# Performance work log

Measured on AMD Instinct MI355X. Metric: run time of the kernel, lower is better.

The kernel has to match this reference:

```python
import math
import jax, jax.numpy as jnp
import numpy as np

B, H, W = 32, 32, 32
SQRT2 = 1.4142  # literal from the torch module


def setup_inputs() -> dict:
    key = jax.random.key(0)
    k1, k2, k3 = jax.random.split(key, 3)
    cost_maps = jax.random.uniform(k1, (B, 1, H, W), jnp.float32, 0.5, 1.5)
    si = jax.random.randint(k2, (B,), 0, H * W)
    gi = jax.random.randint(k3, (B,), 0, H * W)
    gi = jnp.where(gi == si, (gi + 1) % (H * W), gi)
    start_maps = jax.nn.one_hot(si, H * W, dtype=jnp.float32).reshape(B, 1, H, W)
    goal_maps = jax.nn.one_hot(gi, H * W, dtype=jnp.float32).reshape(B, 1, H, W)
    return {"cost_maps": cost_maps, "start_maps": start_maps, "goal_maps": goal_maps}


def _st_softmax_noexp(val):
    # straight-through softmax-without-exp: soft normalize, hard argmax one-hot
    b = val.shape[0]
    v = val.reshape(b, -1)
    y = v / v.sum(-1, keepdims=True)
    ind = jnp.argmax(y, -1)
    y_hard = jax.nn.one_hot(ind, v.shape[-1], dtype=y.dtype)
    y = jax.lax.stop_gradient(y_hard - y) + y
    return y.reshape(val.shape)


def _conv3x3(x, k):
    # x: [B,H,W], k: [3,3]; torch F.conv2d is cross-correlation, as is lax conv
    return jax.lax.conv_general_dilated(x[:, None], k[None, None], (1, 1), ((1, 1), (1, 1)))[:, 0]


def _forward(cost_maps, start_maps, goal_maps, w=1.0):
    cm = cost_maps[:, 0]
    sm = start_maps[:, 0]
    gm = goal_maps[:, 0]
    obs = cm  # obstacles_maps defaults to cost_maps
    b, hgt, wid = cm.shape
    hw = hgt * wid

    # Euclidean heuristic (dis_type='Euc'), scaled by cost map and weight w
    loc = jnp.stack(jnp.meshgrid(jnp.arange(hgt), jnp.arange(wid), indexing='ij'), 0).astype(cm.dtype)  # [2,H,W]
    goal_loc = jnp.einsum('kij,bij->bk', loc, gm)  # [B,2]
    diff = loc.reshape(2, -1)[None] - goal_loc[:, :, None]  # [B,2,HW]
    h = jnp.sqrt((diff ** 2).sum(1)).reshape(b, hgt, wid) * cm * w

    k_s = jnp.array([[1., 1., 1.], [1., 0., 1.], [1., 1., 1.]], cm.dtype)
    k_c = jnp.array([[SQRT2, 1., SQRT2], [1., 0., 1.], [SQRT2, 1., SQRT2]], cm.dtype)
    inv_c = 1.0 / math.sqrt(hw)

    goal_idx = jnp.argmax(gm.reshape(b, -1), -1).astype(cm.dtype)  # [B]
    parents0 = jnp.ones((b, hw), cm.dtype) * goal_idx[:, None]
    bidx = jnp.arange(b)

    def step(carry, t):
        open_m, hist, g, parents, done, tb = carry
        f = g + h
        f_exp = jnp.exp(-f * inv_c) * open_m
        ns = _st_softmax_noexp(f_exp)                        # [B,H,W] node selection
        dist = (ns * gm).sum((1, 2), keepdims=True)
        unsolved = (dist < 1e-8).astype(f.dtype)
        hist_n = jnp.clip(hist + ns, 0.0, 1.0)
        open_n = jnp.clip(open_m - unsolved * ns, 0.0, 1.0)
        neighbor = _conv3x3(ns, k_s) * obs
        g2 = (g * ns).sum((1, 2), keepdims=True) + _conv3x3(ns, k_c)
        idx = ((1.0 - open_n) * (1.0 - hist_n) + open_n * (g > g2).astype(f.dtype)) * neighbor
        idx = jax.lax.stop_gradient(idx)
        g_n = jax.lax.stop_gradient(g2 * idx + g * (1.0 - idx))
        open_n = jax.lax.stop_gradient(jnp.clip(open_n + idx, 0.0, 1.0))
        idxf = idx.reshape(b, -1)
        new_par = jnp.argmax(ns.reshape(b, -1), -1)[:, None].astype(f.dtype)
        parents_n = new_par * idxf + parents * (1.0 - idxf)
        all_solved = jnp.all(unsolved == 0)
        newly = jnp.logical_and(jnp.logical_not(done), all_solved)
        tb_n = jnp.where(newly, t, tb)
        done_n = jnp.logical_or(done, all_solved)
        sel = lambda new, old: jnp.where(done, old, new)  # freeze after torch break
        return (sel(open_n, open_m), sel(hist_n, hist), sel(g_n, g),
                sel(parents_n, parents), done_n, tb_n), None

    carry0 = (sm, jnp.zeros_like(sm), jnp.zeros_like(sm), parents0,
              jnp.array(False), jnp.array(0, jnp.int32))
    (open_f, hist, g, parents, done, tb), _ = jax.lax.scan(
        step, carry0, jnp.arange(hw, dtype=jnp.int32))
    current_t = jnp.where(done, tb, hw - 1)

    # backtrack
    par_i = parents.astype(jnp.int32)
    gm_i = gm.astype(jnp.int32).reshape(b, -1)
    loc0 = (par_i * gm_i).sum(-1)

    def bt_step(c, i):
        path, loc = c
        active = i < current_t
        path = jnp.where(active, path.at[bidx, loc].set(1), path)
        loc = jnp.where(active, par_i[bidx, loc], loc)
        return (path, loc), None

    (path, _), _ = jax.lax.scan(bt_step, (gm_i, loc0), jnp.arange(hw, dtype=jnp.int32))
    path_maps = path.reshape(b, hgt, wid)
    return hist[:, None], path_maps[:, None]


def reference(cost_maps, start_maps, goal_maps):
    return _forward(cost_maps, start_maps, goal_maps)
```

## Files before the change

kernel.cpp:

```cpp
#include <hip/hip_runtime.h>
#include <math.h>

#define HWC 1024
#define NB  32
#define GH  32
#define GW  32
#define NWORD 32
#define NPHASE 30

#define WS_BAR   0
#define WS_SWIN  256
#define WS_STW   (WS_SWIN + NWORD * NB * 4)

#define FEIDX(i) ((((i) & 15) << 6) | ((i) >> 4))

__device__ __forceinline__ float fe_expr(float g, float h, float o) {
    return __fmul_rn(expf(__fmul_rn(__fadd_rn(g, h), -0.03125f)), o);
}

template<int CTRL>
__device__ __forceinline__ float dppmax(float m) {
    int sh = __builtin_amdgcn_update_dpp(__float_as_int(m), __float_as_int(m), CTRL, 0xF, 0xF, false);
    return fmaxf(m, __int_as_float(sh));
}
template<int CTRL>
__device__ __forceinline__ unsigned dppand(unsigned m) {
    int sh = __builtin_amdgcn_update_dpp((int)m, (int)m, CTRL, 0xF, 0xF, false);
    return m & (unsigned)sh;
}

__global__ void dastar_init(unsigned* __restrict__ bar) {
    if (threadIdx.x < 32) bar[threadIdx.x] = 0u;
}

__global__ __launch_bounds__(64)
void dastar_fused(const float* __restrict__ cm_g, const float* __restrict__ sm_g,
                  const float* __restrict__ gm_g, unsigned* __restrict__ swin,
                  unsigned* __restrict__ stw, unsigned* __restrict__ bar,
                  float* __restrict__ out)
{
    const int b   = blockIdx.x;
    const int tid = threadIdx.x;

    __shared__ __align__(16) float feT[HWC];
    __shared__ __align__(16) float gg[HWC], oo[HWC], hi[HWC], cmS[HWC], hhS[HWC];
    __shared__ unsigned slog[HWC * 9];
    __shared__ int goal_sh;

    const float4* cm4 = (const float4*)(cm_g + b * HWC);
    const float4* sm4 = (const float4*)(sm_g + b * HWC);
    const float4* gm4 = (const float4*)(gm_g + b * HWC);
    float cmr[16], oor[16];
#pragma unroll
    for (int q = 0; q < 4; ++q) {
        int i4 = tid * 4 + q;
        float4 c4 = cm4[i4];
        float4 s4 = sm4[i4];
        float4 g4 = gm4[i4];
        int base = i4 * 4;
        float cv[4] = {c4.x, c4.y, c4.z, c4.w};
        float sv[4] = {s4.x, s4.y, s4.z, s4.w};
        float gv[4] = {g4.x, g4.y, g4.z, g4.w};
#pragma unroll
        for (int j = 0; j < 4; ++j) {
            int i = base + j;
            cmr[q * 4 + j] = cv[j];
            oor[q * 4 + j] = sv[j];
            cmS[i] = cv[j];
            gg[i] = 0.0f; hi[i] = 0.0f; oo[i] = sv[j];
            if (gv[j] == 1.0f) goal_sh = i;
        }
    }
    __syncthreads();

    const int   goal = goal_sh;
    const float gy = (float)(goal >> 5), gx = (float)(goal & 31);
#pragma unroll
    for (int k = 0; k < 16; ++k) {
        int i = tid * 16 + k;
        float dy = (float)(i >> 5) - gy;
        float dx = (float)(i & 31) - gx;
        float h  = __fmul_rn(sqrtf(__fadd_rn(__fmul_rn(dy, dy), __fmul_rn(dx, dx))), cmr[k]);
        hhS[i] = h;
        feT[(k << 6) + tid] = fe_expr(0.0f, h, oor[k]);
    }
    __syncthreads();

    const int dyj = tid / 3 - 1, dxj = tid % 3 - 1;
    bool frozen = false, fsolved = false;
    int  fstep = 0;
    int  tstar = HWC - 1;

    float vn[16];
#pragma unroll
    for (int k = 0; k < 16; ++k) vn[k] = feT[(k << 6) + tid];

    int wpub = 0;
    int wred = 0;
    bool done = false;

    for (int phase = 0; phase < NPHASE && !done; ++phase) {
        const int wEnd = (3 + phase < NWORD) ? (3 + phase) : NWORD;

        while (wpub < wEnd) {
            unsigned word;
            if (!frozen) {
                word = 0u;
                const int tbeg = wpub * 32;
                for (int t = tbeg; t < tbeg + 32; ++t) {
                    float v[16];
#pragma unroll
                    for (int k = 0; k < 16; ++k) v[k] = vn[k];
                    const int cbase = tid * 16;
                    float v8[8]; int i8[8];
#pragma unroll
                    for (int k = 0; k < 8; ++k) {
                        bool tk = v[2 * k + 1] > v[2 * k];
                        v8[k] = tk ? v[2 * k + 1] : v[2 * k];
                        i8[k] = cbase + 2 * k + (tk ? 1 : 0);
                    }
                    float v4[4]; int i4a[4];
#pragma unroll
                    for (int k = 0; k < 4; ++k) {
                        bool tk = v8[2 * k + 1] > v8[2 * k];
                        v4[k] = tk ? v8[2 * k + 1] : v8[2 * k];
                        i4a[k] = tk ? i8[2 * k + 1] : i8[2 * k];
                    }
                    float v2[2]; int i2a[2];
#pragma unroll
                    for (int k = 0; k < 2; ++k) {
                        bool tk = v4[2 * k + 1] > v4[2 * k];
                        v2[k] = tk ? v4[2 * k + 1] : v4[2 * k];
                        i2a[k] = tk ? i4a[2 * k + 1] : i4a[2 * k];
                    }
                    bool tk0 = v2[1] > v2[0];
                    float bv = tk0 ? v2[1] : v2[0];
                    int   bi = tk0 ? i2a[1] : i2a[0];

                    float m = bv;
                    m = dppmax<0x111>(m);
                    m = dppmax<0x112>(m);
                    m = dppmax<0x114>(m);
                    m = dppmax<0x118>(m);
                    m = dppmax<0x142>(m);
                    m = dppmax<0x143>(m);
                    float gmax = __int_as_float(__builtin_amdgcn_readlane(__float_as_int(m), 63));
                    unsigned long long bl = __ballot(bv == gmax);
                    int lsel = (int)__ffsll(bl) - 1;
                    if (lsel < 0) lsel = 0;
                    const int  s      = __builtin_amdgcn_readlane(bi, lsel);
                    const bool solved = (s == goal);

                    bool changed = false;
                    float lidx = 0.0f;
                    if (tid < 9) {
                        const int  sy = s >> 5, sx = s & 31;
                        const int  cy = sy + dyj, cx = sx + dxj;
                        const bool ctr = (tid == 4);
                        const bool inb = ctr || (cy >= 0 && cy < GH && cx >= 0 && cx < GW);
                        const int  c  = (cy << 5) | cx;
                        const int  q  = inb ? c : s;
                        const float gq = gg[q], oq = oo[q], hq = hi[q];
                        const float cmq = cmS[q], hhq = hhS[q];
                        const float gs = gg[s];
                        if (ctr) {
                            changed = (hq != 1.0f) || (!solved && oq != 0.0f);
                            hi[s] = 1.0f;
                            if (!solved) { oo[s] = 0.0f; feT[FEIDX(s)] = 0.0f; }
                        } else if (inb) {
                            const float kc = (dyj != 0 && dxj != 0) ? 1.4142f : 1.0f;
                            const float g2 = __fadd_rn(gs, kc);
                            const float t1 = __fmul_rn(__fsub_rn(1.0f, oq), __fsub_rn(1.0f, hq));
                            const float t2 = __fmul_rn(oq, (gq > g2) ? 1.0f : 0.0f);
                            const float idxv = __fmul_rn(__fadd_rn(t1, t2), cmq);
                            lidx = idxv;
                            if (idxv != 0.0f) {
                                changed = true;
                                const float omi = __fsub_rn(1.0f, idxv);
                                const float gn = __fadd_rn(__fmul_rn(g2, idxv), __fmul_rn(gq, omi));
                                const float on = fminf(__fadd_rn(oq, idxv), 1.0f);
                                gg[c] = gn; oo[c] = on;
                                feT[FEIDX(c)] = fe_expr(gn, hhq, on);
                            }
                        }
                        slog[t * 9 + tid] = ctr ? (unsigned)s : __float_as_uint(lidx);
                    }

#pragma unroll
                    for (int k = 0; k < 16; ++k) vn[k] = feT[(k << 6) + tid];

                    unsigned long long chg = __ballot(changed);
                    if (solved) word |= (1u << (t & 31));
                    if (chg == 0ull) {
                        if (solved) word |= ~((1u << (t & 31)) - 1u);
                        frozen = true; fsolved = solved; fstep = t;
                        break;
                    }
                }
            } else {
                word = fsolved ? 0xFFFFFFFFu : 0u;
            }
            if (tid == 0)
                __hip_atomic_store(&swin[wpub * NB + b], word, __ATOMIC_RELEASE, __HIP_MEMORY_SCOPE_AGENT);
            ++wpub;
        }

        if (tid == 0) {
            __hip_atomic_store(&stw[phase * NB + b], frozen ? (fsolved ? 1u : 2u) : 0u,
                               __ATOMIC_RELEASE, __HIP_MEMORY_SCOPE_AGENT);
            __hip_atomic_fetch_add(&bar[phase], 1u, __ATOMIC_ACQ_REL, __HIP_MEMORY_SCOPE_AGENT);
        }
        {
            unsigned guard = 0u;
            while (__hip_atomic_load(&bar[phase], __ATOMIC_ACQUIRE, __HIP_MEMORY_SCOPE_AGENT) < NB) {
                __builtin_amdgcn_s_sleep(1);
                if (++guard > 16000000u) break;
            }
        }

        for (int w = wred; w < wEnd; ++w) {
            unsigned wv = __hip_atomic_load(&swin[w * NB + (tid & 31)], __ATOMIC_ACQUIRE, __HIP_MEMORY_SCOPE_AGENT);
            unsigned A = wv;
            A = dppand<0x111>(A); A = dppand<0x112>(A); A = dppand<0x114>(A);
            A = dppand<0x118>(A); A = dppand<0x142>(A); A = dppand<0x143>(A);
            A = (unsigned)__builtin_amdgcn_readlane((int)A, 63);
            if (A) { tstar = w * 32 + (__ffs(A) - 1); done = true; break; }
        }
        wred = wEnd;
        if (!done) {
            unsigned sv = __hip_atomic_load(&stw[phase * NB + (tid & 31)], __ATOMIC_ACQUIRE, __HIP_MEMORY_SCOPE_AGENT);
            if (__ballot(sv != 0u) == 0xFFFFFFFFFFFFFFFFull) done = true;
        }
    }
    __syncthreads();

    const int Tl = frozen ? min(tstar, fstep) : tstar;

#pragma unroll
    for (int q = 0; q < 4; ++q)
        ((float4*)hi)[tid + (q << 6)] = make_float4(0.f, 0.f, 0.f, 0.f);
    __syncthreads();
    for (int t = tid; t <= Tl; t += 64) hi[(int)slog[t * 9 + 4]] = 1.0f;
    __syncthreads();
#pragma unroll
    for (int q = 0; q < 4; ++q) {
        int i4 = tid + (q << 6);
        ((float4*)(out + b * HWC))[i4] = ((const float4*)hi)[i4];
    }

    const float goalf = (float)goal;
#pragma unroll
    for (int k = 0; k < 16; ++k) {
        int i = tid * 16 + k;
        cmS[i] = goalf;
        hhS[i] = 0.0f;
    }
    __syncthreads();
    if (tid < 9 && tid != 4) {
        for (int t0c = 0; t0c <= Tl; t0c += 16) {
            float iv[16], sv[16];
#pragma unroll
            for (int u = 0; u < 16; ++u) {
                int t = t0c + u;
                if (t <= Tl) {
                    iv[u] = __uint_as_float(slog[t * 9 + tid]);
                    sv[u] = (float)(int)slog[t * 9 + 4];
                } else {
                    iv[u] = 0.0f; sv[u] = 0.0f;
                }
            }
#pragma unroll
            for (int u = 0; u < 16; ++u) {
                if (iv[u] != 0.0f) {
                    int c = (int)sv[u] + (dyj << 5) + dxj;
                    float omi = __fsub_rn(1.0f, iv[u]);
                    cmS[c] = __fadd_rn(__fmul_rn(sv[u], iv[u]), __fmul_rn(cmS[c], omi));
                }
            }
        }
    }
    __syncthreads();

    if (tid == 0) {
        hhS[goal] = 1.0f;
        int loc = (int)cmS[goal];
        for (int i2 = 0; i2 < tstar; ++i2) {
            int w = (loc < 0) ? loc + HWC : loc;
            if (w >= 0 && w < HWC) {
                if (hhS[w] == 1.0f) break;
                hhS[w] = 1.0f;
            }
            int gidx = w < 0 ? 0 : (w > HWC - 1 ? HWC - 1 : w);
            loc = (int)cmS[gidx];
        }
    }
    __syncthreads();
#pragma unroll
    for (int q = 0; q < 4; ++q) {
        int i4 = tid + (q << 6);
        ((float4*)(out + NB * HWC + b * HWC))[i4] = ((const float4*)hhS)[i4];
    }
}

extern "C" void kernel_launch(void* const* d_in, const int* in_sizes, int n_in,
                              void* d_out, int out_size, void* d_ws, size_t ws_size,
                              hipStream_t stream)
{
    const float* cm = (const float*)d_in[0];
    const float* sm = (const float*)d_in[1];
    const float* gm = (const float*)d_in[2];
    float* out = (float*)d_out;

    unsigned* bar  = (unsigned*)((char*)d_ws + WS_BAR);
    unsigned* swin = (unsigned*)((char*)d_ws + WS_SWIN);
    unsigned* stw  = (unsigned*)((char*)d_ws + WS_STW);

    dastar_init<<<1, 64, 0, stream>>>(bar);
    dastar_fused<<<dim3(NB), dim3(64), 0, stream>>>(cm, sm, gm, swin, stw, bar, out);
}
```

Baseline: 132.6 us.

## Use geometric phase bounds for cross-block barriers and vectorized swizzled LDS reads

Replaces the fixed per-word phase schedule (30 phases, each a grid-wide barrier) with 7 phases whose step bounds grow geometrically, so blocks meet at the global atomic barrier far less often. Solved-step words are still published every 32 steps, and the reduction masks each word to the step range of the current phase. Separately, the f-value array in LDS now uses an XOR swizzle so each thread reloads its 16 values with four float4 reads instead of 16 scalar reads. Fewer barriers let fast blocks run further ahead, which may waste steps after the earliest solve. Coarser phases also delay detection of early termination.

```diff
diff --git a/kernel.cpp b/kernel.cpp
--- a/kernel.cpp
+++ b/kernel.cpp
@@ -5,14 +5,13 @@
 #define NB  32
 #define GH  32
 #define GW  32
-#define NWORD 32
-#define NPHASE 30
+#define NPHASE 7
 
 #define WS_BAR   0
 #define WS_SWIN  256
-#define WS_STW   (WS_SWIN + NWORD * NB * 4)
-
-#define FEIDX(i) ((((i) & 15) << 6) | ((i) >> 4))
+#define WS_STW   (WS_SWIN + 32 * NB * 4)
+
+#define FESWZ(i) ((i) ^ (((i) >> 3) & 12))
 
 __device__ __forceinline__ float fe_expr(float g, float h, float o) {
     return __fmul_rn(expf(__fmul_rn(__fadd_rn(g, h), -0.03125f)), o);
@@ -82,127 +81,151 @@
         float dx = (float)(i & 31) - gx;
         float h  = __fmul_rn(sqrtf(__fadd_rn(__fmul_rn(dy, dy), __fmul_rn(dx, dx))), cmr[k]);
         hhS[i] = h;
-        feT[(k << 6) + tid] = fe_expr(0.0f, h, oor[k]);
-    }
-    __syncthreads();
-
+        feT[FESWZ(i)] = fe_expr(0.0f, h, oor[k]);
+    }
+    __syncthreads();
+
+    const int m4 = (tid >> 1) & 3;
     const int dyj = tid / 3 - 1, dxj = tid % 3 - 1;
+
+    float4 vq0, vq1, vq2, vq3;
+    {
+        const float4* f4 = (const float4*)feT;
+        vq0 = f4[(tid << 2) | (0 ^ m4)];
+        vq1 = f4[(tid << 2) | (1 ^ m4)];
+        vq2 = f4[(tid << 2) | (2 ^ m4)];
+        vq3 = f4[(tid << 2) | (3 ^ m4)];
+    }
+
     bool frozen = false, fsolved = false;
-    int  fstep = 0;
-    int  tstar = HWC - 1;
-
-    float vn[16];
-#pragma unroll
-    for (int k = 0; k < 16; ++k) vn[k] = feT[(k << 6) + tid];
-
-    int wpub = 0;
-    int wred = 0;
+    int  fstep = 0, tstar = HWC - 1;
+    unsigned word = 0u;
+    int wpub = 0, t = 0, Pprev = 0;
     bool done = false;
+    const int bounds[NPHASE] = {90, 106, 138, 202, 330, 586, 1024};
 
     for (int phase = 0; phase < NPHASE && !done; ++phase) {
-        const int wEnd = (3 + phase < NWORD) ? (3 + phase) : NWORD;
-
-        while (wpub < wEnd) {
-            unsigned word;
-            if (!frozen) {
-                word = 0u;
-                const int tbeg = wpub * 32;
-                for (int t = tbeg; t < tbeg + 32; ++t) {
-                    float v[16];
-#pragma unroll
-                    for (int k = 0; k < 16; ++k) v[k] = vn[k];
-                    const int cbase = tid * 16;
-                    float v8[8]; int i8[8];
-#pragma unroll
-                    for (int k = 0; k < 8; ++k) {
-                        bool tk = v[2 * k + 1] > v[2 * k];
-                        v8[k] = tk ? v[2 * k + 1] : v[2 * k];
-                        i8[k] = cbase + 2 * k + (tk ? 1 : 0);
-                    }
-                    float v4[4]; int i4a[4];
-#pragma unroll
-                    for (int k = 0; k < 4; ++k) {
-                        bool tk = v8[2 * k + 1] > v8[2 * k];
-                        v4[k] = tk ? v8[2 * k + 1] : v8[2 * k];
-                        i4a[k] = tk ? i8[2 * k + 1] : i8[2 * k];
-                    }
-                    float v2[2]; int i2a[2];
-#pragma unroll
-                    for (int k = 0; k < 2; ++k) {
-                        bool tk = v4[2 * k + 1] > v4[2 * k];
-                        v2[k] = tk ? v4[2 * k + 1] : v4[2 * k];
-                        i2a[k] = tk ? i4a[2 * k + 1] : i4a[2 * k];
-                    }
-                    bool tk0 = v2[1] > v2[0];
-                    float bv = tk0 ? v2[1] : v2[0];
-                    int   bi = tk0 ? i2a[1] : i2a[0];
-
-                    float m = bv;
-                    m = dppmax<0x111>(m);
-                    m = dppmax<0x112>(m);
-                    m = dppmax<0x114>(m);
-                    m = dppmax<0x118>(m);
-                    m = dppmax<0x142>(m);
-                    m = dppmax<0x143>(m);
-                    float gmax = __int_as_float(__builtin_amdgcn_readlane(__float_as_int(m), 63));
-                    unsigned long long bl = __ballot(bv == gmax);
-                    int lsel = (int)__ffsll(bl) - 1;
-                    if (lsel < 0) lsel = 0;
-                    const int  s      = __builtin_amdgcn_readlane(bi, lsel);
-                    const bool solved = (s == goal);
-
-                    bool changed = false;
-                    float lidx = 0.0f;
-                    if (tid < 9) {
-                        const int  sy = s >> 5, sx = s & 31;
-                        const int  cy = sy + dyj, cx = sx + dxj;
-                        const bool ctr = (tid == 4);
-                        const bool inb = ctr || (cy >= 0 && cy < GH && cx >= 0 && cx < GW);
-                        const int  c  = (cy << 5) | cx;
-                        const int  q  = inb ? c : s;
-                        const float gq = gg[q], oq = oo[q], hq = hi[q];
-                        const float cmq = cmS[q], hhq = hhS[q];
-                        const float gs = gg[s];
-                        if (ctr) {
-                            changed = (hq != 1.0f) || (!solved && oq != 0.0f);
-                            hi[s] = 1.0f;
-                            if (!solved) { oo[s] = 0.0f; feT[FEIDX(s)] = 0.0f; }
-                        } else if (inb) {
-                            const float kc = (dyj != 0 && dxj != 0) ? 1.4142f : 1.0f;
-                            const float g2 = __fadd_rn(gs, kc);
-                            const float t1 = __fmul_rn(__fsub_rn(1.0f, oq), __fsub_rn(1.0f, hq));
-                            const float t2 = __fmul_rn(oq, (gq > g2) ? 1.0f : 0.0f);
-                            const float idxv = __fmul_rn(__fadd_rn(t1, t2), cmq);
-                            lidx = idxv;
-                            if (idxv != 0.0f) {
-                                changed = true;
-                                const float omi = __fsub_rn(1.0f, idxv);
-                                const float gn = __fadd_rn(__fmul_rn(g2, idxv), __fmul_rn(gq, omi));
-                                const float on = fminf(__fadd_rn(oq, idxv), 1.0f);
-                                gg[c] = gn; oo[c] = on;
-                                feT[FEIDX(c)] = fe_expr(gn, hhq, on);
-                            }
-                        }
-                        slog[t * 9 + tid] = ctr ? (unsigned)s : __float_as_uint(lidx);
-                    }
-
-#pragma unroll
-                    for (int k = 0; k < 16; ++k) vn[k] = feT[(k << 6) + tid];
-
-                    unsigned long long chg = __ballot(changed);
-                    if (solved) word |= (1u << (t & 31));
-                    if (chg == 0ull) {
-                        if (solved) word |= ~((1u << (t & 31)) - 1u);
-                        frozen = true; fsolved = solved; fstep = t;
-                        break;
+        const int P = bounds[phase];
+
+        while (!frozen && t < P) {
+            float v[16];
+            v[0] = vq0.x; v[1] = vq0.y; v[2] = vq0.z; v[3] = vq0.w;
+            v[4] = vq1.x; v[5] = vq1.y; v[6] = vq1.z; v[7] = vq1.w;
+            v[8] = vq2.x; v[9] = vq2.y; v[10] = vq2.z; v[11] = vq2.w;
+            v[12] = vq3.x; v[13] = vq3.y; v[14] = vq3.z; v[15] = vq3.w;
+            const int cbase = tid * 16;
+            float v8[8]; int i8[8];
+#pragma unroll
+            for (int k = 0; k < 8; ++k) {
+                bool tk = v[2 * k + 1] > v[2 * k];
+                v8[k] = tk ? v[2 * k + 1] : v[2 * k];
+                i8[k] = cbase + 2 * k + (tk ? 1 : 0);
+            }
+            float v4a[4]; int i4a[4];
+#pragma unroll
+            for (int k = 0; k < 4; ++k) {
+                bool tk = v8[2 * k + 1] > v8[2 * k];
+                v4a[k] = tk ? v8[2 * k + 1] : v8[2 * k];
+                i4a[k] = tk ? i8[2 * k + 1] : i8[2 * k];
+            }
+            float v2[2]; int i2a[2];
+#pragma unroll
+            for (int k = 0; k < 2; ++k) {
+                bool tk = v4a[2 * k + 1] > v4a[2 * k];
+                v2[k] = tk ? v4a[2 * k + 1] : v4a[2 * k];
+                i2a[k] = tk ? i4a[2 * k + 1] : i4a[2 * k];
+            }
+            bool tk0 = v2[1] > v2[0];
+            float bv = tk0 ? v2[1] : v2[0];
+            int   bi = tk0 ? i2a[1] : i2a[0];
+
+            float m = bv;
+            m = dppmax<0x111>(m);
+            m = dppmax<0x112>(m);
+            m = dppmax<0x114>(m);
+            m = dppmax<0x118>(m);
+            m = dppmax<0x142>(m);
+            m = dppmax<0x143>(m);
+            float gmax = __int_as_float(__builtin_amdgcn_readlane(__float_as_int(m), 63));
+            unsigned long long bl = __ballot(bv == gmax);
+            int lsel = (int)__ffsll(bl) - 1;
+            if (lsel < 0) lsel = 0;
+            const int  s      = __builtin_amdgcn_readlane(bi, lsel);
+            const bool solved = (s == goal);
+
+            bool changed = false;
+            float lidx = 0.0f;
+            if (tid < 9) {
+                const int  sy = s >> 5, sx = s & 31;
+                const int  cy = sy + dyj, cx = sx + dxj;
+                const bool ctr = (tid == 4);
+                const bool inb = ctr || (cy >= 0 && cy < GH && cx >= 0 && cx < GW);
+                const int  c  = (cy << 5) | cx;
+                const int  q  = inb ? c : s;
+                const float gq = gg[q], oq = oo[q], hq = hi[q];
+                const float cmq = cmS[q], hhq = hhS[q];
+                const float gs = gg[s];
+                if (ctr) {
+                    changed = (hq != 1.0f) || (!solved && oq != 0.0f);
+                    hi[s] = 1.0f;
+                    if (!solved) { oo[s] = 0.0f; feT[FESWZ(s)] = 0.0f; }
+                } else if (inb) {
+                    const float kc = (dyj != 0 && dxj != 0) ? 1.4142f : 1.0f;
+                    const float g2 = __fadd_rn(gs, kc);
+                    const float t1 = __fmul_rn(__fsub_rn(1.0f, oq), __fsub_rn(1.0f, hq));
+                    const float t2 = __fmul_rn(oq, (gq > g2) ? 1.0f : 0.0f);
+                    const float idxv = __fmul_rn(__fadd_rn(t1, t2), cmq);
+                    lidx = idxv;
+                    if (idxv != 0.0f) {
+                        changed = true;
+                        const float omi = __fsub_rn(1.0f, idxv);
+                        const float gn = __fadd_rn(__fmul_rn(g2, idxv), __fmul_rn(gq, omi));
+                        const float on = fminf(__fadd_rn(oq, idxv), 1.0f);
+                        gg[c] = gn; oo[c] = on;
+                        feT[FESWZ(c)] = fe_expr(gn, hhq, on);
                     }
                 }
-            } else {
-                word = fsolved ? 0xFFFFFFFFu : 0u;
-            }
+                slog[t * 9 + tid] = ctr ? (unsigned)s : __float_as_uint(lidx);
+            }
+
+            {
+                const float4* f4 = (const float4*)feT;
+                vq0 = f4[(tid << 2) | (0 ^ m4)];
+                vq1 = f4[(tid << 2) | (1 ^ m4)];
+                vq2 = f4[(tid << 2) | (2 ^ m4)];
+                vq3 = f4[(tid << 2) | (3 ^ m4)];
+            }
+
+            unsigned long long chg = __ballot(changed);
+            if (solved) word |= (1u << (t & 31));
+            if (chg == 0ull) {
+                if (solved) word |= ~((1u << (t & 31)) - 1u);
+                if (tid == 0)
+                    __hip_atomic_store(&swin[wpub * NB + b], word, __ATOMIC_RELEASE, __HIP_MEMORY_SCOPE_AGENT);
+                ++wpub;
+                frozen = true; fsolved = solved; fstep = t;
+                break;
+            }
+            ++t;
+            if ((t & 31) == 0) {
+                if (tid == 0)
+                    __hip_atomic_store(&swin[wpub * NB + b], word, __ATOMIC_RELEASE, __HIP_MEMORY_SCOPE_AGENT);
+                ++wpub; word = 0u;
+            }
+        }
+
+        const int wEnd = (P + 31) >> 5;
+        if (!frozen) {
+            if (t & 31) {
+                if (tid == 0)
+                    __hip_atomic_store(&swin[(t >> 5) * NB + b], word, __ATOMIC_RELEASE, __HIP_MEMORY_SCOPE_AGENT);
+            }
+        } else {
+            unsigned fill = fsolved ? 0xFFFFFFFFu : 0u;
             if (tid == 0)
-                __hip_atomic_store(&swin[wpub * NB + b], word, __ATOMIC_RELEASE, __HIP_MEMORY_SCOPE_AGENT);
-            ++wpub;
+                for (int w = wpub; w < wEnd; ++w)
+                    __hip_atomic_store(&swin[w * NB + b], fill, __ATOMIC_RELEASE, __HIP_MEMORY_SCOPE_AGENT);
+            if (wpub < wEnd) wpub = wEnd;
         }
 
         if (tid == 0) {
@@ -218,15 +241,20 @@
             }
         }
 
-        for (int w = wred; w < wEnd; ++w) {
+        for (int w = (Pprev >> 5); w < wEnd; ++w) {
+            int lo = Pprev - 32 * w; if (lo < 0) lo = 0;
+            int hi2 = P - 32 * w;    if (hi2 > 32) hi2 = 32;
+            unsigned mask = (hi2 == 32 ? 0xFFFFFFFFu : ((1u << hi2) - 1u))
+                          & ~(lo == 0 ? 0u : ((1u << lo) - 1u));
             unsigned wv = __hip_atomic_load(&swin[w * NB + (tid & 31)], __ATOMIC_ACQUIRE, __HIP_MEMORY_SCOPE_AGENT);
             unsigned A = wv;
             A = dppand<0x111>(A); A = dppand<0x112>(A); A = dppand<0x114>(A);
             A = dppand<0x118>(A); A = dppand<0x142>(A); A = dppand<0x143>(A);
             A = (unsigned)__builtin_amdgcn_readlane((int)A, 63);
+            A &= mask;
             if (A) { tstar = w * 32 + (__ffs(A) - 1); done = true; break; }
         }
-        wred = wEnd;
+        Pprev = P;
         if (!done) {
             unsigned sv = __hip_atomic_load(&stw[phase * NB + (tid & 31)], __ATOMIC_ACQUIRE, __HIP_MEMORY_SCOPE_AGENT);
             if (__ballot(sv != 0u) == 0xFFFFFFFFFFFFFFFFull) done = true;
@@ -240,7 +268,7 @@
     for (int q = 0; q < 4; ++q)
         ((float4*)hi)[tid + (q << 6)] = make_float4(0.f, 0.f, 0.f, 0.f);
     __syncthreads();
-    for (int t = tid; t <= Tl; t += 64) hi[(int)slog[t * 9 + 4]] = 1.0f;
+    for (int tt = tid; tt <= Tl; tt += 64) hi[(int)slog[tt * 9 + 4]] = 1.0f;
     __syncthreads();
 #pragma unroll
     for (int q = 0; q < 4; ++q) {
@@ -261,10 +289,10 @@
             float iv[16], sv[16];
 #pragma unroll
             for (int u = 0; u < 16; ++u) {
-                int t = t0c + u;
-                if (t <= Tl) {
-                    iv[u] = __uint_as_float(slog[t * 9 + tid]);
-                    sv[u] = (float)(int)slog[t * 9 + 4];
+                int tt = t0c + u;
+                if (tt <= Tl) {
+                    iv[u] = __uint_as_float(slog[tt * 9 + tid]);
+                    sv[u] = (float)(int)slog[tt * 9 + 4];
                 } else {
                     iv[u] = 0.0f; sv[u] = 0.0f;
                 }
```

Result: slower. 146.4 us (+10.4%).

## Use geometric phase bounds for cross-block barrier and simplify argmax selection

Applied to the files above, without the earlier changes.

Replaces the fixed one-word-per-phase barrier schedule (30 phases) with 7 phases whose step bounds start at 90 and then grow geometrically, so fewer grid-wide barriers run when the search terminates early. The argmax is restructured into a plain fmax tree plus an equality mask to recover the index, which cuts select instructions. The frozen/changed-detection logic and its stw status array are removed, so every block keeps stepping until the global all-solved step is found. This can mean extra wasted steps when termination falls just past a bound.

```diff
diff --git a/kernel.cpp b/kernel.cpp
--- a/kernel.cpp
+++ b/kernel.cpp
@@ -5,12 +5,10 @@
 #define NB  32
 #define GH  32
 #define GW  32
-#define NWORD 32
-#define NPHASE 30
+#define NPHASE 7
 
 #define WS_BAR   0
 #define WS_SWIN  256
-#define WS_STW   (WS_SWIN + NWORD * NB * 4)
 
 #define FEIDX(i) ((((i) & 15) << 6) | ((i) >> 4))
 
@@ -36,8 +34,7 @@
 __global__ __launch_bounds__(64)
 void dastar_fused(const float* __restrict__ cm_g, const float* __restrict__ sm_g,
                   const float* __restrict__ gm_g, unsigned* __restrict__ swin,
-                  unsigned* __restrict__ stw, unsigned* __restrict__ bar,
-                  float* __restrict__ out)
+                  unsigned* __restrict__ bar, float* __restrict__ out)
 {
     const int b   = blockIdx.x;
     const int tid = threadIdx.x;
@@ -87,129 +84,103 @@
     __syncthreads();
 
     const int dyj = tid / 3 - 1, dxj = tid % 3 - 1;
-    bool frozen = false, fsolved = false;
-    int  fstep = 0;
+
+    float vn[16];
+#pragma unroll
+    for (int k = 0; k < 16; ++k) vn[k] = feT[(k << 6) + tid];
+
     int  tstar = HWC - 1;
-
-    float vn[16];
-#pragma unroll
-    for (int k = 0; k < 16; ++k) vn[k] = feT[(k << 6) + tid];
-
-    int wpub = 0;
-    int wred = 0;
+    unsigned word = 0u;
+    int wpub = 0, t = 0, Pprev = 0;
     bool done = false;
+    const int bounds[NPHASE] = {90, 106, 138, 202, 330, 586, 1024};
 
     for (int phase = 0; phase < NPHASE && !done; ++phase) {
-        const int wEnd = (3 + phase < NWORD) ? (3 + phase) : NWORD;
-
-        while (wpub < wEnd) {
-            unsigned word;
-            if (!frozen) {
-                word = 0u;
-                const int tbeg = wpub * 32;
-                for (int t = tbeg; t < tbeg + 32; ++t) {
-                    float v[16];
-#pragma unroll
-                    for (int k = 0; k < 16; ++k) v[k] = vn[k];
-                    const int cbase = tid * 16;
-                    float v8[8]; int i8[8];
-#pragma unroll
-                    for (int k = 0; k < 8; ++k) {
-                        bool tk = v[2 * k + 1] > v[2 * k];
-                        v8[k] = tk ? v[2 * k + 1] : v[2 * k];
-                        i8[k] = cbase + 2 * k + (tk ? 1 : 0);
+        const int P = bounds[phase];
+
+        while (t < P) {
+            float v[16];
+#pragma unroll
+            for (int k = 0; k < 16; ++k) v[k] = vn[k];
+
+            float a0 = fmaxf(v[0], v[1]),  a1 = fmaxf(v[2], v[3]);
+            float a2 = fmaxf(v[4], v[5]),  a3 = fmaxf(v[6], v[7]);
+            float a4 = fmaxf(v[8], v[9]),  a5 = fmaxf(v[10], v[11]);
+            float a6 = fmaxf(v[12], v[13]), a7 = fmaxf(v[14], v[15]);
+            float b0 = fmaxf(a0, a1), b1 = fmaxf(a2, a3);
+            float b2 = fmaxf(a4, a5), b3 = fmaxf(a6, a7);
+            float vmax = fmaxf(fmaxf(b0, b1), fmaxf(b2, b3));
+
+            float m = vmax;
+            m = dppmax<0x111>(m);
+            m = dppmax<0x112>(m);
+            m = dppmax<0x114>(m);
+            m = dppmax<0x118>(m);
+            m = dppmax<0x142>(m);
+            m = dppmax<0x143>(m);
+            const float gmax = __int_as_float(__builtin_amdgcn_readlane(__float_as_int(m), 63));
+
+            unsigned msk = 0u;
+#pragma unroll
+            for (int k = 0; k < 16; ++k) msk |= (v[k] == gmax) ? (1u << k) : 0u;
+            const int lft = __ffs(msk) - 1;
+            unsigned long long bl = __ballot(msk != 0u);
+            int lsel = (int)__ffsll(bl) - 1;
+            if (lsel < 0) lsel = 0;
+            const int  s      = __builtin_amdgcn_readlane(tid * 16 + lft, lsel);
+            const bool solved = (s == goal);
+
+            if (tid < 9) {
+                const int sy = s >> 5, sx = s & 31;
+                if (tid == 4) {
+                    hi[s] = 1.0f;
+                    if (!solved) { oo[s] = 0.0f; feT[FEIDX(s)] = 0.0f; }
+                    slog[t * 9 + 4] = (unsigned)s;
+                } else {
+                    const int  cy = sy + dyj, cx = sx + dxj;
+                    const bool inb = (cy >= 0 && cy < GH && cx >= 0 && cx < GW);
+                    const int  c  = (cy << 5) | cx;
+                    const int  q  = inb ? c : s;
+                    const float gq = gg[q], oq = oo[q], hq = hi[q];
+                    const float cmq = cmS[q], hhq = hhS[q];
+                    const float gs = gg[s];
+                    float lidx = 0.0f;
+                    if (inb) {
+                        const float kc = (dyj != 0 && dxj != 0) ? 1.4142f : 1.0f;
+                        const float g2 = __fadd_rn(gs, kc);
+                        const float t1 = __fmul_rn(__fsub_rn(1.0f, oq), __fsub_rn(1.0f, hq));
+                        const float t2 = __fmul_rn(oq, (gq > g2) ? 1.0f : 0.0f);
+                        const float idxv = __fmul_rn(__fadd_rn(t1, t2), cmq);
+                        lidx = idxv;
+                        if (idxv != 0.0f) {
+                            const float omi = __fsub_rn(1.0f, idxv);
+                            const float gn = __fadd_rn(__fmul_rn(g2, idxv), __fmul_rn(gq, omi));
+                            const float on = fminf(__fadd_rn(oq, idxv), 1.0f);
+                            gg[c] = gn; oo[c] = on;
+                            feT[FEIDX(c)] = fe_expr(gn, hhq, on);
+                        }
                     }
-                    float v4[4]; int i4a[4];
-#pragma unroll
-                    for (int k = 0; k < 4; ++k) {
-                        bool tk = v8[2 * k + 1] > v8[2 * k];
-                        v4[k] = tk ? v8[2 * k + 1] : v8[2 * k];
-                        i4a[k] = tk ? i8[2 * k + 1] : i8[2 * k];
-                    }
-                    float v2[2]; int i2a[2];
-#pragma unroll
-                    for (int k = 0; k < 2; ++k) {
-                        bool tk = v4[2 * k + 1] > v4[2 * k];
-                        v2[k] = tk ? v4[2 * k + 1] : v4[2 * k];
-                        i2a[k] = tk ? i4a[2 * k + 1] : i4a[2 * k];
-                    }
-                    bool tk0 = v2[1] > v2[0];
-                    float bv = tk0 ? v2[1] : v2[0];
-                    int   bi = tk0 ? i2a[1] : i2a[0];
-
-                    float m = bv;
-                    m = dppmax<0x111>(m);
-                    m = dppmax<0x112>(m);
-                    m = dppmax<0x114>(m);
-                    m = dppmax<0x118>(m);
-                    m = dppmax<0x142>(m);
-                    m = dppmax<0x143>(m);
-                    float gmax = __int_as_float(__builtin_amdgcn_readlane(__float_as_int(m), 63));
-                    unsigned long long bl = __ballot(bv == gmax);
-                    int lsel = (int)__ffsll(bl) - 1;
-                    if (lsel < 0) lsel = 0;
-                    const int  s      = __builtin_amdgcn_readlane(bi, lsel);
-                    const bool solved = (s == goal);
-
-                    bool changed = false;
-                    float lidx = 0.0f;
-                    if (tid < 9) {
-                        const int  sy = s >> 5, sx = s & 31;
-                        const int  cy = sy + dyj, cx = sx + dxj;
-                        const bool ctr = (tid == 4);
-                        const bool inb = ctr || (cy >= 0 && cy < GH && cx >= 0 && cx < GW);
-                        const int  c  = (cy << 5) | cx;
-                        const int  q  = inb ? c : s;
-                        const float gq = gg[q], oq = oo[q], hq = hi[q];
-                        const float cmq = cmS[q], hhq = hhS[q];
-                        const float gs = gg[s];
-                        if (ctr) {
-                            changed = (hq != 1.0f) || (!solved && oq != 0.0f);
-                            hi[s] = 1.0f;
-                            if (!solved) { oo[s] = 0.0f; feT[FEIDX(s)] = 0.0f; }
-                        } else if (inb) {
-                            const float kc = (dyj != 0 && dxj != 0) ? 1.4142f : 1.0f;
-                            const float g2 = __fadd_rn(gs, kc);
-                            const float t1 = __fmul_rn(__fsub_rn(1.0f, oq), __fsub_rn(1.0f, hq));
-                            const float t2 = __fmul_rn(oq, (gq > g2) ? 1.0f : 0.0f);
-                            const float idxv = __fmul_rn(__fadd_rn(t1, t2), cmq);
-                            lidx = idxv;
-                            if (idxv != 0.0f) {
-                                changed = true;
-                                const float omi = __fsub_rn(1.0f, idxv);
-                                const float gn = __fadd_rn(__fmul_rn(g2, idxv), __fmul_rn(gq, omi));
-                                const float on = fminf(__fadd_rn(oq, idxv), 1.0f);
-                                gg[c] = gn; oo[c] = on;
-                                feT[FEIDX(c)] = fe_expr(gn, hhq, on);
-                            }
-                        }
-                        slog[t * 9 + tid] = ctr ? (unsigned)s : __float_as_uint(lidx);
-                    }
-
-#pragma unroll
-                    for (int k = 0; k < 16; ++k) vn[k] = feT[(k << 6) + tid];
-
-                    unsigned long long chg = __ballot(changed);
-                    if (solved) word |= (1u << (t & 31));
-                    if (chg == 0ull) {
-                        if (solved) word |= ~((1u << (t & 31)) - 1u);
-                        frozen = true; fsolved = solved; fstep = t;
-                        break;
-                    }
+                    slog[t * 9 + tid] = __float_as_uint(lidx);
                 }
-            } else {
-                word = fsolved ? 0xFFFFFFFFu : 0u;
-            }
-            if (tid == 0)
-                __hip_atomic_store(&swin[wpub * NB + b], word, __ATOMIC_RELEASE, __HIP_MEMORY_SCOPE_AGENT);
-            ++wpub;
-        }
-
-        if (tid == 0) {
-            __hip_atomic_store(&stw[phase * NB + b], frozen ? (fsolved ? 1u : 2u) : 0u,
-                               __ATOMIC_RELEASE, __HIP_MEMORY_SCOPE_AGENT);
+            }
+
+#pragma unroll
+            for (int k = 0; k < 16; ++k) vn[k] = feT[(k << 6) + tid];
+
+            if (solved) word |= (1u << (t & 31));
+            ++t;
+            if ((t & 31) == 0) {
+                if (tid == 0)
+                    __hip_atomic_store(&swin[wpub * NB + b], word, __ATOMIC_RELEASE, __HIP_MEMORY_SCOPE_AGENT);
+                ++wpub; word = 0u;
+            }
+        }
+
+        if ((t & 31) && tid == 0)
+            __hip_atomic_store(&swin[(t >> 5) * NB + b], word, __ATOMIC_RELEASE, __HIP_MEMORY_SCOPE_AGENT);
+
+        if (tid == 0)
             __hip_atomic_fetch_add(&bar[phase], 1u, __ATOMIC_ACQ_REL, __HIP_MEMORY_SCOPE_AGENT);
-        }
         {
             unsigned guard = 0u;
             while (__hip_atomic_load(&bar[phase], __ATOMIC_ACQUIRE, __HIP_MEMORY_SCOPE_AGENT) < NB) {
@@ -218,29 +189,31 @@
             }
         }
 
-        for (int w = wred; w < wEnd; ++w) {
+        const int wEnd = (P + 31) >> 5;
+        for (int w = (Pprev >> 5); w < wEnd; ++w) {
+            int lo = Pprev - 32 * w; if (lo < 0) lo = 0;
+            int hi2 = P - 32 * w;    if (hi2 > 32) hi2 = 32;
+            unsigned mask = (hi2 == 32 ? 0xFFFFFFFFu : ((1u << hi2) - 1u))
+                          & ~(lo == 0 ? 0u : ((1u << lo) - 1u));
             unsigned wv = __hip_atomic_load(&swin[w * NB + (tid & 31)], __ATOMIC_ACQUIRE, __HIP_MEMORY_SCOPE_AGENT);
             unsigned A = wv;
             A = dppand<0x111>(A); A = dppand<0x112>(A); A = dppand<0x114>(A);
             A = dppand<0x118>(A); A = dppand<0x142>(A); A = dppand<0x143>(A);
             A = (unsigned)__builtin_amdgcn_readlane((int)A, 63);
+            A &= mask;
             if (A) { tstar = w * 32 + (__ffs(A) - 1); done = true; break; }
         }
-        wred = wEnd;
-        if (!done) {
-            unsigned sv = __hip_atomic_load(&stw[phase * NB + (tid & 31)], __ATOMIC_ACQUIRE, __HIP_MEMORY_SCOPE_AGENT);
-            if (__ballot(sv != 0u) == 0xFFFFFFFFFFFFFFFFull) done = true;
-        }
-    }
-    __syncthreads();
-
-    const int Tl = frozen ? min(tstar, fstep) : tstar;
+        Pprev = P;
+    }
+    __syncthreads();
+
+    const int Tl = tstar;
 
 #pragma unroll
     for (int q = 0; q < 4; ++q)
         ((float4*)hi)[tid + (q << 6)] = make_float4(0.f, 0.f, 0.f, 0.f);
     __syncthreads();
-    for (int t = tid; t <= Tl; t += 64) hi[(int)slog[t * 9 + 4]] = 1.0f;
+    for (int tt = tid; tt <= Tl; tt += 64) hi[(int)slog[tt * 9 + 4]] = 1.0f;
     __syncthreads();
 #pragma unroll
     for (int q = 0; q < 4; ++q) {
@@ -261,10 +234,10 @@
             float iv[16], sv[16];
 #pragma unroll
             for (int u = 0; u < 16; ++u) {
-                int t = t0c + u;
-                if (t <= Tl) {
-                    iv[u] = __uint_as_float(slog[t * 9 + tid]);
-                    sv[u] = (float)(int)slog[t * 9 + 4];
+                int tt = t0c + u;
+                if (tt <= Tl) {
+                    iv[u] = __uint_as_float(slog[tt * 9 + tid]);
+                    sv[u] = (float)(int)slog[tt * 9 + 4];
                 } else {
                     iv[u] = 0.0f; sv[u] = 0.0f;
                 }
@@ -313,8 +286,7 @@
 
     unsigned* bar  = (unsigned*)((char*)d_ws + WS_BAR);
     unsigned* swin = (unsigned*)((char*)d_ws + WS_SWIN);
-    unsigned* stw  = (unsigned*)((char*)d_ws + WS_STW);
 
     dastar_init<<<1, 64, 0, stream>>>(bar);
-    dastar_fused<<<dim3(NB), dim3(64), 0, stream>>>(cm, sm, gm, swin, stw, bar, out);
-}
+    dastar_fused<<<dim3(NB), dim3(64), 0, stream>>>(cm, sm, gm, swin, bar, out);
+}
```

Result: faster. 115.6 us (-12.8%).
